# Performance work log

Measured on AMD Instinct MI355X. Metric: run time of the kernel, lower is better.

Reference implementation:

```python
import jax, jax.numpy as jnp
import numpy as np

B, H, L, D = 2, 16, 2048, 64


def setup_inputs() -> dict:
    key = jax.random.key(0)
    kq, kk, kv = jax.random.split(key, 3)
    return {
        "query": jax.random.normal(kq, (B, H, L, D), dtype=jnp.float32),
        "key": jax.random.normal(kk, (B, H, L, D), dtype=jnp.float32),
        "value": jax.random.normal(kv, (B, H, L, D), dtype=jnp.float32),
        "dhead": D,
        "causal": 1,
    }


def reference(query, key, value, dhead, causal):
    # mode='dhead': muP attention with scale 1/dhead (not 1/sqrt(dhead)).
    # Inputs/outputs in [B, H, L, D] layout (the torch code transposes to
    # [B, L, H, D] for the einsum and transposes back; net layout is the same).
    scale = 1.0 / dhead
    a = jnp.einsum('bhld,bhLd->bhlL', query, key) * scale  # [B,H,L,L]
    if causal:
        seq = a.shape[-1]
        mask = jnp.tril(jnp.ones((seq, seq), dtype=bool))  # [L,L]
        a = jnp.where(mask, a, jnp.float32(-jnp.inf))
    a = jax.nn.softmax(a, axis=-1)
    out = jnp.einsum('bhlL,bhLd->bhld', a, value)  # [B,H,L,D]
    return out
```

## Files before the change

### kernel.cpp

```cpp
#include <hip/hip_runtime.h>

#define BHH 32
#define SEQ 2048
#define DH 64
#define BQ 64
#define BK 64
#define NKT (SEQ / BK)
#define NQB (SEQ / BQ)
#define NT  (BHH * NKT)
#define TCH 8
#define NCH 80
#define NMULTI 72

typedef __attribute__((ext_vector_type(8))) _Float16 half8_t;
typedef __attribute__((ext_vector_type(4))) _Float16 half4_t;
typedef __attribute__((ext_vector_type(4))) float f32x4;

__device__ __forceinline__ void async_copy16(const void* g, const void* lds) {
    __builtin_amdgcn_global_load_lds(
        (const __attribute__((address_space(1))) unsigned int*)g,
        (__attribute__((address_space(3))) unsigned int*)lds, 16, 0, 0);
}

__device__ __forceinline__ void chunk_map(int cid, int& qb, int& s) {
    if (cid < 8)       { qb = 8 + cid;              s = 0; }
    else if (cid < 24) { qb = 16 + (cid - 8) / 2;   s = (cid - 8) & 1; }
    else if (cid < 48) { qb = 24 + (cid - 24) / 3;  s = (cid - 24) % 3; }
    else { const int u = cid - 48; qb = (7 - (u >> 2)) + 8 * (u & 3); s = qb >> 3; }
}
__device__ __forceinline__ int pidx_of(int qb, int s) {
    return (qb < 16) ? (qb - 8) * 2 + s
         : (qb < 24) ? 16 + (qb - 16) * 3 + s
         :             40 + (qb - 24) * 4 + s;
}

__global__ __launch_bounds__(256) void prep_kv(const float* __restrict__ K,
                                               const float* __restrict__ V,
                                               _Float16* __restrict__ Kf,
                                               _Float16* __restrict__ Vf) {
    __shared__ _Float16 l[64 * 76];
    const int t = threadIdx.x;
    const int wave = t >> 6, lane = t & 63, ln15 = lane & 15, quad = lane >> 4;
    const int row = t >> 2, col0 = (t & 3) * 16;
    int b = blockIdx.x;

    if (b < NT) {
        const float4* src = (const float4*)(K + (size_t)b * 4096 + row * 64 + col0);
        #pragma unroll
        for (int q = 0; q < 2; ++q) {
            float4 f0 = src[q * 2], f1 = src[q * 2 + 1];
            half8_t w = { (_Float16)f0.x, (_Float16)f0.y, (_Float16)f0.z, (_Float16)f0.w,
                          (_Float16)f1.x, (_Float16)f1.y, (_Float16)f1.z, (_Float16)f1.w };
            *(half8_t*)&l[row * 72 + col0 + q * 8] = w;
        }
        __syncthreads();
        #pragma unroll
        for (int p = 0; p < 2; ++p) {
            const int bid = wave * 2 + p, c = bid >> 1, k0 = bid & 1;
            half8_t w = *(const half8_t*)&l[(c * 16 + ln15) * 72 + k0 * 32 + quad * 8];
            *(half8_t*)&Kf[(size_t)b * 4096 + bid * 512 + lane * 8] = w;
        }
    } else {
        b -= NT;
        const float4* src = (const float4*)(V + (size_t)b * 4096 + row * 64 + col0);
        #pragma unroll
        for (int q = 0; q < 4; ++q) {
            float4 f = src[q];
            half4_t w = { (_Float16)f.x, (_Float16)f.y, (_Float16)f.z, (_Float16)f.w };
            *(half4_t*)&l[row * 76 + col0 + q * 4] = w;
        }
        __syncthreads();
        #pragma unroll
        for (int p = 0; p < 4; ++p) {
            const int f = wave * 4 + p, cn = f >> 2, c = f & 3;
            half4_t w;
            #pragma unroll
            for (int j = 0; j < 4; ++j)
                w[j] = l[(c * 16 + quad * 4 + j) * 76 + cn * 16 + ln15];
            *(half4_t*)&Vf[(size_t)b * 4096 + f * 256 + lane * 4] = w;
        }
    }
}

__global__ __launch_bounds__(256) void fattn_kernel(
        const float* __restrict__ Q, const _Float16* __restrict__ Kf,
        const _Float16* __restrict__ Vf, float* __restrict__ O,
        _Float16* __restrict__ Opart, float* __restrict__ Lpart) {
    const int bh  = blockIdx.x & 31;
    const int cid = blockIdx.x >> 5;
    int qb, s;
    chunk_map(cid, qb, s);
    const int nc  = (qb >> 3) + 1;
    const int len = min(TCH, qb + 1 - s * TCH);
    const int kt0 = s * TCH;

    const int tid  = threadIdx.x;
    const int wave = tid >> 6;
    const int lane = tid & 63;
    const int ln15 = lane & 15;
    const int quad = lane >> 4;

    __shared__ _Float16 ldsK[2][4096];
    __shared__ _Float16 ldsV[2][4096];

    const size_t base = (size_t)bh * SEQ * DH;
    const int q0   = qb * BQ;
    const int qrow = q0 + wave * 16;

    const float qscale = 1.44269504f / 64.0f;
    half8_t qfrag[2];
    {
        const float* qp = Q + base + (size_t)(qrow + ln15) * DH + quad * 8;
        #pragma unroll
        for (int k0 = 0; k0 < 2; ++k0) {
            float4 a = *(const float4*)(qp + k0 * 32);
            float4 b = *(const float4*)(qp + k0 * 32 + 4);
            qfrag[k0] = (half8_t){
                (_Float16)(a.x * qscale), (_Float16)(a.y * qscale),
                (_Float16)(a.z * qscale), (_Float16)(a.w * qscale),
                (_Float16)(b.x * qscale), (_Float16)(b.y * qscale),
                (_Float16)(b.z * qscale), (_Float16)(b.w * qscale) };
        }
    }

    f32x4 acc[4] = {};
    float l_i = 0.f;
    const size_t tb = (size_t)(bh * NKT) * 4096;

    #define STAGE(kt_, b_) do {                                              \
        const size_t toff = tb + (size_t)(kt_) * 4096;                       \
        _Pragma("unroll")                                                    \
        for (int i_ = 0; i_ < 4; ++i_) {                                     \
            const int bid_ = wave * 4 + i_;                                  \
            if (bid_ < 8)                                                    \
                async_copy16(Kf + toff + bid_ * 512 + lane * 8,              \
                             &ldsK[b_][bid_ * 512]);                         \
            else                                                             \
                async_copy16(Vf + toff + (bid_ - 8) * 512 + lane * 8,        \
                             &ldsV[b_][(bid_ - 8) * 512]);                   \
        }                                                                    \
    } while (0)

    STAGE(kt0, 0);
    __syncthreads();

    for (int i = 0; i < len; ++i) {
        const int kt = kt0 + i;
        const _Float16* kvk = ldsK[i & 1];
        const _Float16* kvv = ldsV[i & 1];
        if (i + 1 < len) STAGE(kt + 1, (i + 1) & 1);

        f32x4 st[4];
        #pragma unroll
        for (int c = 0; c < 4; ++c) {
            half8_t kf0 = *(const half8_t*)&kvk[(c * 2 + 0) * 512 + lane * 8];
            half8_t kf1 = *(const half8_t*)&kvk[(c * 2 + 1) * 512 + lane * 8];
            f32x4 a = {};
            a = __builtin_amdgcn_mfma_f32_16x16x32_f16(kf0, qfrag[0], a, 0, 0, 0);
            a = __builtin_amdgcn_mfma_f32_16x16x32_f16(kf1, qfrag[1], a, 0, 0, 0);
            st[c] = a;
        }

        const int kbase = kt * BK;
        const bool needmask = (kt == qb);
        const int rowi = qrow + ln15;
        half4_t pfrag[4];
        float psum = 0.f;
        #pragma unroll
        for (int c = 0; c < 4; ++c) {
            #pragma unroll
            for (int rr = 0; rr < 4; ++rr) {
                float v = __builtin_amdgcn_exp2f(st[c][rr]);
                if (needmask && (kbase + c * 16 + quad * 4 + rr) > rowi) v = 0.f;
                pfrag[c][rr] = (_Float16)v;
                psum += v;
            }
        }
        psum += __shfl_xor(psum, 16);
        psum += __shfl_xor(psum, 32);
        l_i += psum;

        #pragma unroll
        for (int cn = 0; cn < 4; ++cn) {
            #pragma unroll
            for (int c = 0; c < 4; ++c) {
                half4_t vf = *(const half4_t*)&kvv[(cn * 4 + c) * 256 + lane * 4];
                acc[cn] = __builtin_amdgcn_mfma_f32_16x16x16f16(vf, pfrag[c], acc[cn], 0, 0, 0);
            }
        }
        __syncthreads();
    }

    if (nc == 1) {
        const float rl = 1.0f / l_i;
        float* op = O + base + (size_t)(qrow + ln15) * DH;
        #pragma unroll
        for (int cn = 0; cn < 4; ++cn) {
            float4 o;
            o.x = acc[cn][0] * rl;
            o.y = acc[cn][1] * rl;
            o.z = acc[cn][2] * rl;
            o.w = acc[cn][3] * rl;
            *(float4*)(op + cn * 16 + quad * 4) = o;
        }
    } else {
        const int pidx = pidx_of(qb, s);
        const int row = wave * 16 + ln15;
        _Float16* pp = Opart + ((size_t)bh * NMULTI + pidx) * 4096 + row * 64;
        #pragma unroll
        for (int cn = 0; cn < 4; ++cn) {
            half4_t h = { (_Float16)acc[cn][0], (_Float16)acc[cn][1],
                          (_Float16)acc[cn][2], (_Float16)acc[cn][3] };
            *(half4_t*)(pp + cn * 16 + quad * 4) = h;
        }
        if (quad == 0)
            Lpart[((size_t)bh * NMULTI + pidx) * 64 + row] = l_i;
    }
    #undef STAGE
}

__global__ __launch_bounds__(256) void combine_kernel(
        const _Float16* __restrict__ Opart, const float* __restrict__ Lpart,
        float* __restrict__ O) {
    const int bh = blockIdx.x & 31;
    const int qb = 8 + (blockIdx.x >> 5);
    const int nc = (qb >> 3) + 1;
    const int pbase = pidx_of(qb, 0);
    const int t = threadIdx.x;
    const int row = t >> 2, col0 = (t & 3) * 16;

    const _Float16* P = Opart + ((size_t)bh * NMULTI + pbase) * 4096 + row * 64 + col0;
    const float* Lp = Lpart + ((size_t)bh * NMULTI + pbase) * 64 + row;

    float acc[16] = {};
    float l = 0.f;
    for (int c = 0; c < nc; ++c) {
        l += Lp[c * 64];
        half8_t a = *(const half8_t*)(P + c * 4096);
        half8_t b = *(const half8_t*)(P + c * 4096 + 8);
        #pragma unroll
        for (int j = 0; j < 8; ++j) { acc[j] += (float)a[j]; acc[8 + j] += (float)b[j]; }
    }
    const float rl = 1.0f / l;
    float* op = O + ((size_t)bh * SEQ + qb * 64 + row) * DH + col0;
    #pragma unroll
    for (int v = 0; v < 4; ++v) {
        float4 o = { acc[v * 4] * rl, acc[v * 4 + 1] * rl,
                     acc[v * 4 + 2] * rl, acc[v * 4 + 3] * rl };
        *(float4*)(op + v * 4) = o;
    }
}

extern "C" void kernel_launch(void* const* d_in, const int* in_sizes, int n_in,
                              void* d_out, int out_size, void* d_ws, size_t ws_size,
                              hipStream_t stream) {
    const float* Q = (const float*)d_in[0];
    const float* K = (const float*)d_in[1];
    const float* V = (const float*)d_in[2];
    float* O = (float*)d_out;
    char* ws = (char*)d_ws;
    _Float16* Kf    = (_Float16*)ws;
    _Float16* Vf    = (_Float16*)(ws + ((size_t)8 << 20));
    _Float16* Opart = (_Float16*)(ws + ((size_t)16 << 20));
    float*    Lpart = (float*)(ws + ((size_t)16 << 20)
                               + (size_t)BHH * NMULTI * 4096 * 2);

    prep_kv<<<2 * NT, 256, 0, stream>>>(K, V, Kf, Vf);
    fattn_kernel<<<NCH * BHH, 256, 0, stream>>>(Q, Kf, Vf, O, Opart, Lpart);
    combine_kernel<<<24 * BHH, 256, 0, stream>>>(Opart, Lpart, O);
}
```

Measured before the change: 136.2 us.

## Double query tile to 128 rows so each wave reuses K/V for two row groups

Raises the query block from 64 to 128 rows, with each wave now computing two 16-row groups against every staged K/V tile. Each LDS K/V fragment feeds twice as many MFMAs, which halves global and LDS traffic per query. The split-KV chunk map, the partial-output layout and the combine kernel are rebuilt for 128-row blocks and 36 partial slots. In exchange the grid has half as many blocks, register pressure is higher, and some fully masked diagonal work is wasted per wave.

```diff
diff --git a/kernel.cpp b/kernel.cpp
--- a/kernel.cpp
+++ b/kernel.cpp
@@ -3,14 +3,13 @@
 #define BHH 32
 #define SEQ 2048
 #define DH 64
-#define BQ 64
+#define BQ 128
 #define BK 64
 #define NKT (SEQ / BK)
-#define NQB (SEQ / BQ)
 #define NT  (BHH * NKT)
 #define TCH 8
-#define NCH 80
-#define NMULTI 72
+#define NCH 40
+#define NMULTI 36
 
 typedef __attribute__((ext_vector_type(8))) _Float16 half8_t;
 typedef __attribute__((ext_vector_type(4))) _Float16 half4_t;
@@ -23,15 +22,15 @@
 }
 
 __device__ __forceinline__ void chunk_map(int cid, int& qb, int& s) {
-    if (cid < 8)       { qb = 8 + cid;              s = 0; }
-    else if (cid < 24) { qb = 16 + (cid - 8) / 2;   s = (cid - 8) & 1; }
-    else if (cid < 48) { qb = 24 + (cid - 24) / 3;  s = (cid - 24) % 3; }
-    else { const int u = cid - 48; qb = (7 - (u >> 2)) + 8 * (u & 3); s = qb >> 3; }
+    if (cid < 4)       { qb = 4 + cid;                    s = 0; }
+    else if (cid < 12) { const int u = cid - 4;  qb = 8 + (u >> 1); s = u & 1; }
+    else if (cid < 24) { const int u = cid - 12; qb = 12 + u / 3;   s = u % 3; }
+    else { const int u = cid - 24; qb = (3 - (u >> 2)) + 4 * (u & 3); s = qb >> 2; }
 }
 __device__ __forceinline__ int pidx_of(int qb, int s) {
-    return (qb < 16) ? (qb - 8) * 2 + s
-         : (qb < 24) ? 16 + (qb - 16) * 3 + s
-         :             40 + (qb - 24) * 4 + s;
+    return (qb < 8) ? (qb - 4) * 2 + s
+         : (qb < 12) ? 8 + (qb - 8) * 3 + s
+         :             20 + (qb - 12) * 4 + s;
 }
 
 __global__ __launch_bounds__(256) void prep_kv(const float* __restrict__ K,
@@ -90,8 +89,9 @@
     const int cid = blockIdx.x >> 5;
     int qb, s;
     chunk_map(cid, qb, s);
-    const int nc  = (qb >> 3) + 1;
-    const int len = min(TCH, qb + 1 - s * TCH);
+    const int nc  = (qb >> 2) + 1;
+    const int nt  = 2 * qb + 2;
+    const int len = min(TCH, nt - s * TCH);
     const int kt0 = s * TCH;
 
     const int tid  = threadIdx.x;
@@ -104,18 +104,19 @@
     __shared__ _Float16 ldsV[2][4096];
 
     const size_t base = (size_t)bh * SEQ * DH;
-    const int q0   = qb * BQ;
-    const int qrow = q0 + wave * 16;
+    const int q0 = qb * BQ;
+    const int qw = q0 + wave * 32;
 
     const float qscale = 1.44269504f / 64.0f;
-    half8_t qfrag[2];
-    {
-        const float* qp = Q + base + (size_t)(qrow + ln15) * DH + quad * 8;
+    half8_t qfrag[2][2];
+    #pragma unroll
+    for (int g = 0; g < 2; ++g) {
+        const float* qp = Q + base + (size_t)(qw + g * 16 + ln15) * DH + quad * 8;
         #pragma unroll
         for (int k0 = 0; k0 < 2; ++k0) {
             float4 a = *(const float4*)(qp + k0 * 32);
             float4 b = *(const float4*)(qp + k0 * 32 + 4);
-            qfrag[k0] = (half8_t){
+            qfrag[g][k0] = (half8_t){
                 (_Float16)(a.x * qscale), (_Float16)(a.y * qscale),
                 (_Float16)(a.z * qscale), (_Float16)(a.w * qscale),
                 (_Float16)(b.x * qscale), (_Float16)(b.y * qscale),
@@ -123,8 +124,8 @@
         }
     }
 
-    f32x4 acc[4] = {};
-    float l_i = 0.f;
+    f32x4 acc[2][4] = {};
+    float l_i[2] = {0.f, 0.f};
     const size_t tb = (size_t)(bh * NKT) * 4096;
 
     #define STAGE(kt_, b_) do {                                              \
@@ -150,71 +151,84 @@
         const _Float16* kvv = ldsV[i & 1];
         if (i + 1 < len) STAGE(kt + 1, (i + 1) & 1);
 
-        f32x4 st[4];
+        f32x4 st[2][4];
         #pragma unroll
         for (int c = 0; c < 4; ++c) {
             half8_t kf0 = *(const half8_t*)&kvk[(c * 2 + 0) * 512 + lane * 8];
             half8_t kf1 = *(const half8_t*)&kvk[(c * 2 + 1) * 512 + lane * 8];
-            f32x4 a = {};
-            a = __builtin_amdgcn_mfma_f32_16x16x32_f16(kf0, qfrag[0], a, 0, 0, 0);
-            a = __builtin_amdgcn_mfma_f32_16x16x32_f16(kf1, qfrag[1], a, 0, 0, 0);
-            st[c] = a;
+            #pragma unroll
+            for (int g = 0; g < 2; ++g) {
+                f32x4 a = {};
+                a = __builtin_amdgcn_mfma_f32_16x16x32_f16(kf0, qfrag[g][0], a, 0, 0, 0);
+                a = __builtin_amdgcn_mfma_f32_16x16x32_f16(kf1, qfrag[g][1], a, 0, 0, 0);
+                st[g][c] = a;
+            }
         }
 
         const int kbase = kt * BK;
-        const bool needmask = (kt == qb);
-        const int rowi = qrow + ln15;
-        half4_t pfrag[4];
-        float psum = 0.f;
-        #pragma unroll
-        for (int c = 0; c < 4; ++c) {
-            #pragma unroll
-            for (int rr = 0; rr < 4; ++rr) {
-                float v = __builtin_amdgcn_exp2f(st[c][rr]);
-                if (needmask && (kbase + c * 16 + quad * 4 + rr) > rowi) v = 0.f;
-                pfrag[c][rr] = (_Float16)v;
-                psum += v;
-            }
-        }
-        psum += __shfl_xor(psum, 16);
-        psum += __shfl_xor(psum, 32);
-        l_i += psum;
+        half4_t pfrag[2][4];
+        #pragma unroll
+        for (int g = 0; g < 2; ++g) {
+            const bool needmask = (kbase + 63) > (qw + g * 16);
+            const int rowi = qw + g * 16 + ln15;
+            float psum = 0.f;
+            #pragma unroll
+            for (int c = 0; c < 4; ++c) {
+                #pragma unroll
+                for (int rr = 0; rr < 4; ++rr) {
+                    float v = __builtin_amdgcn_exp2f(st[g][c][rr]);
+                    if (needmask && (kbase + c * 16 + quad * 4 + rr) > rowi) v = 0.f;
+                    pfrag[g][c][rr] = (_Float16)v;
+                    psum += v;
+                }
+            }
+            psum += __shfl_xor(psum, 16);
+            psum += __shfl_xor(psum, 32);
+            l_i[g] += psum;
+        }
 
         #pragma unroll
         for (int cn = 0; cn < 4; ++cn) {
             #pragma unroll
             for (int c = 0; c < 4; ++c) {
                 half4_t vf = *(const half4_t*)&kvv[(cn * 4 + c) * 256 + lane * 4];
-                acc[cn] = __builtin_amdgcn_mfma_f32_16x16x16f16(vf, pfrag[c], acc[cn], 0, 0, 0);
+                acc[0][cn] = __builtin_amdgcn_mfma_f32_16x16x16f16(vf, pfrag[0][c], acc[0][cn], 0, 0, 0);
+                acc[1][cn] = __builtin_amdgcn_mfma_f32_16x16x16f16(vf, pfrag[1][c], acc[1][cn], 0, 0, 0);
             }
         }
         __syncthreads();
     }
 
     if (nc == 1) {
-        const float rl = 1.0f / l_i;
-        float* op = O + base + (size_t)(qrow + ln15) * DH;
-        #pragma unroll
-        for (int cn = 0; cn < 4; ++cn) {
-            float4 o;
-            o.x = acc[cn][0] * rl;
-            o.y = acc[cn][1] * rl;
-            o.z = acc[cn][2] * rl;
-            o.w = acc[cn][3] * rl;
-            *(float4*)(op + cn * 16 + quad * 4) = o;
+        #pragma unroll
+        for (int g = 0; g < 2; ++g) {
+            const float rl = 1.0f / l_i[g];
+            float* op = O + base + (size_t)(qw + g * 16 + ln15) * DH;
+            #pragma unroll
+            for (int cn = 0; cn < 4; ++cn) {
+                float4 o;
+                o.x = acc[g][cn][0] * rl;
+                o.y = acc[g][cn][1] * rl;
+                o.z = acc[g][cn][2] * rl;
+                o.w = acc[g][cn][3] * rl;
+                *(float4*)(op + cn * 16 + quad * 4) = o;
+            }
         }
     } else {
         const int pidx = pidx_of(qb, s);
-        const int row = wave * 16 + ln15;
-        _Float16* pp = Opart + ((size_t)bh * NMULTI + pidx) * 4096 + row * 64;
-        #pragma unroll
-        for (int cn = 0; cn < 4; ++cn) {
-            half4_t h = { (_Float16)acc[cn][0], (_Float16)acc[cn][1],
-                          (_Float16)acc[cn][2], (_Float16)acc[cn][3] };
-            *(half4_t*)(pp + cn * 16 + quad * 4) = h;
-        }
-        if (quad == 0)
-            Lpart[((size_t)bh * NMULTI + pidx) * 64 + row] = l_i;
+        #pragma unroll
+        for (int g = 0; g < 2; ++g) {
+            const int row = wave * 32 + g * 16 + ln15;
+            _Float16* pp = Opart + ((size_t)bh * NMULTI + pidx) * 8192 + row * 64;
+            #pragma unroll
+            for (int cn = 0; cn < 4; ++cn) {
+                half4_t h = { (_Float16)acc[g][cn][0], (_Float16)acc[g][cn][1],
+                              (_Float16)acc[g][cn][2], (_Float16)acc[g][cn][3] };
+                *(half4_t*)(pp + cn * 16 + quad * 4) = h;
+            }
+            if (quad == 0)
+                Lpart[((size_t)bh * NMULTI + pidx) * 128 + row] = l_i[g];
+        }
     }
     #undef STAGE
 }
@@ -223,28 +237,30 @@
         const _Float16* __restrict__ Opart, const float* __restrict__ Lpart,
         float* __restrict__ O) {
     const int bh = blockIdx.x & 31;
-    const int qb = 8 + (blockIdx.x >> 5);
-    const int nc = (qb >> 3) + 1;
+    const int qb = 4 + (blockIdx.x >> 5);
+    const int nc = (qb >> 2) + 1;
     const int pbase = pidx_of(qb, 0);
     const int t = threadIdx.x;
-    const int row = t >> 2, col0 = (t & 3) * 16;
-
-    const _Float16* P = Opart + ((size_t)bh * NMULTI + pbase) * 4096 + row * 64 + col0;
-    const float* Lp = Lpart + ((size_t)bh * NMULTI + pbase) * 64 + row;
-
-    float acc[16] = {};
+    const int row = t >> 1, col0 = (t & 1) * 32;
+
+    const _Float16* P = Opart + ((size_t)bh * NMULTI + pbase) * 8192 + row * 64 + col0;
+    const float* Lp = Lpart + ((size_t)bh * NMULTI + pbase) * 128 + row;
+
+    float acc[32] = {};
     float l = 0.f;
     for (int c = 0; c < nc; ++c) {
-        l += Lp[c * 64];
-        half8_t a = *(const half8_t*)(P + c * 4096);
-        half8_t b = *(const half8_t*)(P + c * 4096 + 8);
-        #pragma unroll
-        for (int j = 0; j < 8; ++j) { acc[j] += (float)a[j]; acc[8 + j] += (float)b[j]; }
+        l += Lp[c * 128];
+        #pragma unroll
+        for (int v = 0; v < 4; ++v) {
+            half8_t a = *(const half8_t*)(P + c * 8192 + v * 8);
+            #pragma unroll
+            for (int j = 0; j < 8; ++j) acc[v * 8 + j] += (float)a[j];
+        }
     }
     const float rl = 1.0f / l;
-    float* op = O + ((size_t)bh * SEQ + qb * 64 + row) * DH + col0;
+    float* op = O + ((size_t)bh * SEQ + qb * 128 + row) * DH + col0;
     #pragma unroll
-    for (int v = 0; v < 4; ++v) {
+    for (int v = 0; v < 8; ++v) {
         float4 o = { acc[v * 4] * rl, acc[v * 4 + 1] * rl,
                      acc[v * 4 + 2] * rl, acc[v * 4 + 3] * rl };
         *(float4*)(op + v * 4) = o;
@@ -263,9 +279,9 @@
     _Float16* Vf    = (_Float16*)(ws + ((size_t)8 << 20));
     _Float16* Opart = (_Float16*)(ws + ((size_t)16 << 20));
     float*    Lpart = (float*)(ws + ((size_t)16 << 20)
-                               + (size_t)BHH * NMULTI * 4096 * 2);
+                               + (size_t)BHH * NMULTI * 8192 * 2);
 
     prep_kv<<<2 * NT, 256, 0, stream>>>(K, V, Kf, Vf);
     fattn_kernel<<<NCH * BHH, 256, 0, stream>>>(Q, Kf, Vf, O, Opart, Lpart);
-    combine_kernel<<<24 * BHH, 256, 0, stream>>>(Opart, Lpart, O);
-}
+    combine_kernel<<<12 * BHH, 256, 0, stream>>>(Opart, Lpart, O);
+}
```

Measured after the change: 140.5 us. +3.2%, slower.
